# Kernel tuning notes

Measured on AMD Instinct MI355X. Metric: run time of the kernel, lower is better.

The kernel has to match this reference:

```python
import math
import jax, jax.numpy as jnp
import numpy as np
from jax import lax

jax.config.update("jax_enable_x64", True)

DECOMP_LEVEL = 5
# Daubechies-5 (db5) decomposition low-pass filter (pywt convention)
_DB5_LO = np.array([0.003335725285001549, -0.012580751999015526, -0.006241490213011705,
                    0.07757149384006515, -0.03224486958502952, -0.24229488706619015,
                    0.13842814590110342, 0.7243085284385744, 0.6038292697974729,
                    0.160102397974125], dtype=np.float64)
_L = _DB5_LO.size
_DB5_HI = _DB5_LO[::-1].copy() * ((-1.0) ** np.arange(_L))  # QMF high-pass
LO = jnp.asarray(_DB5_LO, jnp.float32)
HI = jnp.asarray(_DB5_HI, jnp.float32)
LOR = jnp.asarray(_DB5_LO[::-1].copy(), jnp.float32)
HIR = jnp.asarray(_DB5_HI[::-1].copy(), jnp.float32)


def _an_last(x):
    # orthonormal periodized analysis along last axis: (..., n) -> (..., n/2) x2
    n = x.shape[-1]
    lead = x.shape[:-1]
    xp = jnp.concatenate([x, x[..., : _L - 2]], axis=-1).reshape(-1, 1, n + _L - 2)
    k = jnp.stack([LO, HI])[:, None, :]  # (2,1,L)
    y = lax.conv_general_dilated(xp, k, (2,), "VALID")  # (B,2,n/2)
    y = y.reshape(lead + (2, n // 2))
    return y[..., 0, :], y[..., 1, :]


def _syn_last(a, d):
    # exact transpose/inverse of _an_last (orthonormal -> W^T = W^-1)
    n2 = a.shape[-1]
    n = 2 * n2
    lead = a.shape[:-1]
    B = int(np.prod(lead)) if lead else 1
    u = jnp.zeros((B, 2, n), a.dtype)
    u = u.at[:, 0, ::2].set(a.reshape(B, n2))
    u = u.at[:, 1, ::2].set(d.reshape(B, n2))
    up = jnp.concatenate([u[..., -(_L - 1):], u], axis=-1)  # circular left pad
    k = jnp.stack([LOR, HIR])[None, :, :]  # (1,2,L)
    y = lax.conv_general_dilated(up, k, (1,), "VALID")  # (B,1,n)
    return y.reshape(lead + (n,))


def _dwt2(x):  # x: (C,h,w) -> ll, lh, hl, hh each (C,h/2,w/2)
    a_h, d_h = _an_last(x.swapaxes(-1, -2))
    a_h = a_h.swapaxes(-1, -2)
    d_h = d_h.swapaxes(-1, -2)
    ll, lh = _an_last(a_h)
    hl, hh = _an_last(d_h)
    return ll, lh, hl, hh


def _idwt2(ll, lh, hl, hh):
    a_h = _syn_last(ll, lh)
    d_h = _syn_last(hl, hh)
    return _syn_last(a_h.swapaxes(-1, -2), d_h.swapaxes(-1, -2)).swapaxes(-1, -2)


def _estimate_noise(data):
    p = data.shape[0]
    rr = data @ data.T
    rri = jnp.linalg.inv(rr + 1e-6 * jnp.eye(p, dtype=data.dtype))
    def per_band(i):
        xx = rri - jnp.outer(rri[:, i], rri[i, :]) / rri[i, i]
        beta = xx @ rr[:, i]
        return beta.at[i].set(0.0)
    betas = jax.vmap(per_band)(jnp.arange(p))  # (p,p)
    return data - betas @ data


def hyres_forward(x):
    H, W, K = x.shape
    N = H * W
    data = x.reshape(N, K).T.astype(jnp.float64)
    w = _estimate_noise(data)
    omega1 = (jnp.sqrt(jnp.var(w, axis=1, ddof=1)) + 1e-30) ** 2  # (K,) f64
    y_w = x * omega1 ** -0.5  # whitened, f64
    u, s, v_pca = jnp.linalg.svd(y_w.reshape(N, K), full_matrices=False)
    pc = (u * s).reshape(W, H, K).astype(jnp.float32).transpose(2, 0, 1)  # (K,H,W)
    # multi-level 2D DWT per channel
    ll = pc
    highs = []
    for _ in range(DECOMP_LEVEL):
        ll, lh, hl, hh = _dwt2(ll)
        highs.append((lh, hl, hh))
    # overwrite-style full coefficient image [[LL,LH],[HL,HH]] recursively
    full = ll
    for lh, hl, hh in reversed(highs):
        top = jnp.concatenate([full, lh], axis=-1)
        bot = jnp.concatenate([hl, hh], axis=-1)
        full = jnp.concatenate([top, bot], axis=-2)
    V = full.transpose(1, 2, 0).reshape(N, K)
    V2 = V * V
    norm_v = jnp.sum(V2)
    n_xyz = jnp.asarray(V.size, jnp.float32)
    col_norm = jnp.sum(V2, axis=0)  # (K,)
    # SURE of soft-threshold over a 15-point grid in [0, sqrt(log N)]
    ts = np.linspace(0.0, math.sqrt(math.log(N)), 15).astype(np.float32)
    sure_cols = []
    for t in ts:
        t2 = float(t * t)
        s_t = (jnp.sum(jnp.minimum(V2, t2), axis=0)
               + 2.0 * jnp.sum((V2 > t2).astype(jnp.float32), axis=0)
               - col_norm)
        sure_cols.append(s_t)
    sure_all = jnp.stack(sure_cols, axis=1)  # (K,15)
    c_const = norm_v - n_xyz
    # replicate the in-place cumulative update: S_r = sum_{j<r} S_j + sure_r + C
    def step(acc, sure_r):
        s_r = acc + sure_r + c_const
        return acc + s_r, jnp.min(s_r)
    _, min_sure = lax.scan(step, jnp.zeros((15,), jnp.float32), sure_all)
    # early-exit: first rank>1 where min_sure increases; else loop ends at K-1
    cond = min_sure[2:] > min_sure[1:-1]
    rank = jnp.where(jnp.any(cond), 2 + jnp.argmax(cond), K - 1)
    mask = (jnp.arange(K) < rank).astype(jnp.float32)[:, None, None]
    # truncation-to-rank == zeroing channels >= rank (inverse DWT is linear)
    y = ll * mask
    for lh, hl, hh in reversed(highs):
        y = _idwt2(y, lh * mask, hl * mask, hh * mask)
    y_est = y.transpose(1, 2, 0).reshape(N, K)  # zero cols beyond rank
    out = (omega1.astype(jnp.float32) ** 0.5) * (y_est @ v_pca.astype(jnp.float32)).reshape(H, W, K)
    return out


def setup_inputs() -> dict:
    key = jax.random.key(0)
    k1, k2, k3 = jax.random.split(key, 3)
    H = W = 384
    K = 191
    R = 8  # low-rank spectral structure + noise, as HyRes assumes
    a = jax.random.normal(k1, (H * W, R), jnp.float32)
    b = jax.random.normal(k2, (R, K), jnp.float32)
    x = (a @ b) / np.sqrt(R) + 0.1 * jax.random.normal(k3, (H * W, K), jnp.float32)
    return {"x": x.reshape(H, W, K)}


def reference(x):
    return hyres_forward(x)
```

## Files before the change

### kernel.cpp

```cpp
#include <hip/hip_runtime.h>
#include <math.h>

#define K_     191
#define LD     192
#define N_     147456
#define MSUB   16
#define NT     15
#define TRI_N  18336
#define SMEM_CHOL  ((TRI_N + 1056) * 8)
#define SMEM_SOLVE ((TRI_N + 192 + 192 + 192) * 8)
#define SMEM2_SZ (6880 * 8 + 32 * 4 + TRI_N * 4)

#define NPAIR  6
#define NSPLIT 256
#define CHUNK  (N_ / NSPLIT)
#define RSTEP  16

__constant__ float c_lo[10] = {
  0.003335725285001549f, -0.012580751999015526f, -0.006241490213011705f,
  0.07757149384006515f,  -0.03224486958502952f, -0.24229488706619015f,
  0.13842814590110342f,   0.7243085284385744f,   0.6038292697974729f,
  0.160102397974125f };
__constant__ float c_hi[10] = {
  0.160102397974125f,    -0.6038292697974729f,   0.7243085284385744f,
 -0.13842814590110342f,  -0.24229488706619015f,  0.03224486958502952f,
  0.07757149384006515f,   0.006241490213011705f,-0.012580751999015526f,
 -0.003335725285001549f };

__global__ __launch_bounds__(256, 6) void k_rr(const float* __restrict__ x,
                                               double* __restrict__ rrg,
                                               double* __restrict__ m)
{
  __shared__ float Asf[2][RSTEP][64];
  __shared__ float Bsf[2][RSTEP][64];

  const int bid   = blockIdx.x;
  const int split = bid & (NSPLIT - 1);
  const int pair  = bid >> 8;
  const int BI[6] = {0, 0, 0, 1, 1, 2};
  const int BJ[6] = {0, 1, 2, 1, 2, 2};
  const int bi = BI[pair], bj = BJ[pair];
  const int diag = (bi == bj);
  const int ca = bi * 64, cb = bj * 64;

  const int t  = threadIdx.x;
  const int tx = t & 15, ty = t >> 4;
  const int mycol = t & 63, rowgrp = t >> 6;
  const long n0 = (long)split * CHUNK;

  double acc[4][4];
  #pragma unroll
  for (int v = 0; v < 4; ++v)
    #pragma unroll
    for (int u = 0; u < 4; ++u) acc[v][u] = 0.0;
  double csum = 0.0;

  float ra[4], rbv[4];
  const int cA = ca + mycol, cB = cb + mycol;
  const bool okA = (cA < K_), okB = (cB < K_);

  auto LOADT = [&](int r0) {
    #pragma unroll
    for (int i = 0; i < 4; ++i) {
      int row = i * 4 + rowgrp;
      long gr = (n0 + r0 + row) * (long)K_;
      float va = okA ? x[gr + cA] : 0.f;
      ra[i] = va;
      if (diag) csum += (double)va;
      else      rbv[i] = okB ? x[gr + cB] : 0.f;
    }
  };
  auto WRITET = [&](int buf) {
    #pragma unroll
    for (int i = 0; i < 4; ++i) {
      int row = i * 4 + rowgrp;
      Asf[buf][row][mycol] = ra[i];
      if (!diag) Bsf[buf][row][mycol] = rbv[i];
    }
  };

  LOADT(0);
  WRITET(0);
  __syncthreads();

  int cur = 0;
  for (int r0 = 0; r0 < CHUNK; r0 += RSTEP) {
    const bool hasnext = (r0 + RSTEP < CHUNK);
    if (hasnext) LOADT(r0 + RSTEP);
    const float (*As)[64] = Asf[cur];
    const float (*Bs)[64] = diag ? Asf[cur] : Bsf[cur];
    #pragma unroll 4
    for (int k = 0; k < RSTEP; ++k) {
      double a0 = (double)As[k][ty],      a1 = (double)As[k][ty + 16];
      double a2 = (double)As[k][ty + 32], a3 = (double)As[k][ty + 48];
      double b0 = (double)Bs[k][tx],      b1 = (double)Bs[k][tx + 16];
      double b2 = (double)Bs[k][tx + 32], b3 = (double)Bs[k][tx + 48];
      acc[0][0] += a0 * b0; acc[0][1] += a0 * b1; acc[0][2] += a0 * b2; acc[0][3] += a0 * b3;
      acc[1][0] += a1 * b0; acc[1][1] += a1 * b1; acc[1][2] += a1 * b2; acc[1][3] += a1 * b3;
      acc[2][0] += a2 * b0; acc[2][1] += a2 * b1; acc[2][2] += a2 * b2; acc[2][3] += a2 * b3;
      acc[3][0] += a3 * b0; acc[3][1] += a3 * b1; acc[3][2] += a3 * b2; acc[3][3] += a3 * b3;
    }
    if (hasnext) WRITET(cur ^ 1);
    __syncthreads();
    cur ^= 1;
  }

  #pragma unroll
  for (int v = 0; v < 4; ++v) {
    int mrow = ca + ty + 16 * v;
    #pragma unroll
    for (int u = 0; u < 4; ++u) {
      int ncol = cb + tx + 16 * u;
      if (mrow < K_ && ncol < K_)
        atomicAdd(&rrg[(size_t)mrow * K_ + ncol], acc[v][u]);
    }
  }

  if (diag) {
    double* sc = (double*)Bsf;
    sc[t] = csum;
    __syncthreads();
    if (t < 64) {
      int c = ca + t;
      if (c < K_) {
        double s = sc[t] + sc[t + 64] + sc[t + 128] + sc[t + 192];
        atomicAdd(&m[c], s);
      }
    }
  }
}

__global__ __launch_bounds__(256) void k_reduce(const double* __restrict__ rrg,
                                                double* __restrict__ rr)
{
  int idx = blockIdx.x * 256 + threadIdx.x;
  if (idx >= TRI_N) return;
  int i = (int)((sqrtf(8.f * (float)idx + 1.f) - 1.f) * 0.5f);
  while ((i + 1) * (i + 2) / 2 <= idx) ++i;
  while (i * (i + 1) / 2 > idx) --i;
  int j = idx - (i * (i + 1)) / 2;
  double s = rrg[(size_t)j * K_ + i];
  rr[i * LD + j] = s;
  rr[j * LD + i] = s;
}

__global__ __launch_bounds__(512) void k_chol(
    const double* __restrict__ rr, double* __restrict__ Lg,
    double* __restrict__ rdg)
{
  extern __shared__ double smem[];
  double* tri = smem;
  double* tmp = smem + TRI_N;
  const int t = threadIdx.x;

  for (int i = t >> 5; i < K_; i += 16) {
    int base = (i * (i + 1)) / 2;
    for (int j = t & 31; j <= i; j += 32) {
      double v = rr[i * LD + j];
      tri[base + j] = (i == j) ? v + 1e-6 : v;
    }
  }
  __syncthreads();

  for (int J = 0; J < 6; ++J) {
    const int j0 = J * 32;
    const int nb = (K_ - j0 < 32) ? (K_ - j0) : 32;

    if (t < 64) {
      const int rl = t & 31;
      double a[32];
      #pragma unroll
      for (int c = 0; c < 32; ++c) {
        int i = j0 + rl;
        a[c] = (c <= rl && rl < nb) ? tri[(i * (i + 1)) / 2 + j0 + c] : 0.0;
      }
      #pragma unroll
      for (int k = 0; k < 32; ++k) {
        double akk = __shfl(a[k], k);
        double piv = sqrt(akk);
        double inv = 1.0 / piv;
        if (t == k) {
          tmp[k] = inv;
          if (j0 + k < K_) rdg[j0 + k] = inv;
        }
        a[k] = (rl == k) ? piv : a[k] * inv;
        #pragma unroll
        for (int c = k + 1; c < 32; ++c) {
          double lck = __shfl(a[k], c);
          if (c <= rl) a[c] -= a[k] * lck;
        }
      }
      if (t < 32 && rl < nb) {
        int i = j0 + rl;
        int rb = (i * (i + 1)) / 2 + j0;
        #pragma unroll
        for (int c = 0; c < 32; ++c)
          if (c <= rl) tri[rb + c] = a[c];
      }
    }
    __syncthreads();

    {
      int p = j0 + 32 + t;
      if (nb == 32 && p < K_) {
        int pb = (p * (p + 1)) / 2 + j0;
        double v[32];
        #pragma unroll
        for (int c = 0; c < 32; ++c) v[c] = tri[pb + c];
        #pragma unroll
        for (int c = 0; c < 32; ++c) {
          double s = v[c];
          #pragma unroll
          for (int q = 0; q < c; ++q) {
            int cc = j0 + c;
            s -= v[q] * tri[(cc * (cc + 1)) / 2 + j0 + q];
          }
          v[c] = s * tmp[c];
        }
        #pragma unroll
        for (int c = 0; c < 32; ++c) tri[pb + c] = v[c];
      }
    }
    __syncthreads();

    {
      int s0 = j0 + 32;
      int n = K_ - s0;
      if (n > 0) {
        int R4 = (n + 3) >> 2;
        int T4 = R4 * (R4 + 1) / 2;
        for (int tile = t; tile < T4; tile += 512) {
          int ti = (int)((sqrtf(8.f * (float)tile + 1.f) - 1.f) * 0.5f);
          while ((ti + 1) * (ti + 2) / 2 <= tile) ++ti;
          while (ti * (ti + 1) / 2 > tile) --ti;
          int tj = tile - ti * (ti + 1) / 2;
          int r0 = s0 + ti * 4, c0 = s0 + tj * 4;
          int rb[4], cb[4];
          #pragma unroll
          for (int u = 0; u < 4; ++u) {
            int r = (r0 + u < K_) ? r0 + u : K_ - 1;
            rb[u] = (r * (r + 1)) / 2;
            int c = (c0 + u < K_) ? c0 + u : K_ - 1;
            cb[u] = (c * (c + 1)) / 2;
          }
          double acc[4][4];
          #pragma unroll
          for (int u = 0; u < 4; ++u)
            #pragma unroll
            for (int v2 = 0; v2 < 4; ++v2) acc[u][v2] = 0.0;
          #pragma unroll 4
          for (int p = 0; p < 32; ++p) {
            double lr[4], lc[4];
            #pragma unroll
            for (int u = 0; u < 4; ++u) {
              lr[u] = tri[rb[u] + j0 + p];
              lc[u] = tri[cb[u] + j0 + p];
            }
            #pragma unroll
            for (int u = 0; u < 4; ++u)
              #pragma unroll
              for (int v2 = 0; v2 < 4; ++v2) acc[u][v2] += lr[u] * lc[v2];
          }
          #pragma unroll
          for (int u = 0; u < 4; ++u) {
            int r = r0 + u;
            if (r < K_) {
              #pragma unroll
              for (int v2 = 0; v2 < 4; ++v2) {
                int c = c0 + v2;
                if (c <= r) tri[rb[u] + c] -= acc[u][v2];
              }
            }
          }
        }
      }
    }
    __syncthreads();
  }

  for (int idx = t; idx < TRI_N; idx += 512) Lg[idx] = tri[idx];
}

__global__ __launch_bounds__(256) void k_csolve(
    const double* __restrict__ Lg, const double* __restrict__ rdg,
    const double* __restrict__ mg, double* __restrict__ s2g,
    double* __restrict__ zg)
{
  extern __shared__ double ssm[];
  double* Ls   = ssm;
  double* rd_s = Ls + TRI_N;
  double* m_sh = rd_s + 192;
  double* ys   = m_sh + 192;
  const int t = threadIdx.x;
  const int bid = blockIdx.x;

  const int start = (bid < K_) ? (bid * (bid + 1)) / 2 : 0;
  for (int idx = start + t; idx < TRI_N; idx += 256) Ls[idx] = Lg[idx];
  if (t < K_) { rd_s[t] = rdg[t]; m_sh[t] = mg[t]; }
  __syncthreads();

  if (t >= 64) return;
  const int l = t;

  if (bid < K_) {
    const int i = bid;
    double x0 = 0.0, x1 = 0.0, x2 = 0.0;
    {
      double rdi = rd_s[i];
      if ((i & 63) == l) {
        int sl = i >> 6;
        if (sl == 0) x0 = rdi; else if (sl == 1) x1 = rdi; else x2 = rdi;
      }
    }
    for (int r = i + 1; r < K_; ++r) {
      int rb = (r * (r + 1)) >> 1;
      double partial = 0.0;
      { int k = l;       if (k < r) partial += Ls[rb + k] * x0; }
      { int k = l + 64;  if (k < r) partial += Ls[rb + k] * x1; }
      { int k = l + 128; if (k < r) partial += Ls[rb + k] * x2; }
      #pragma unroll
      for (int mm = 32; mm > 0; mm >>= 1) partial += __shfl_xor(partial, mm);
      double val = -partial * rd_s[r];
      if ((r & 63) == l) {
        int sl = r >> 6;
        if (sl == 0) x0 = val; else if (sl == 1) x1 = val; else x2 = val;
      }
    }
    double s2p = x0 * x0 + x1 * x1 + x2 * x2;
    #pragma unroll
    for (int mm = 32; mm > 0; mm >>= 1) s2p += __shfl_xor(s2p, mm);
    if (l == 0) s2g[i] = s2p;
  } else {
    double y0 = 0.0, y1 = 0.0, y2 = 0.0;
    for (int r = 0; r < K_; ++r) {
      int rb = (r * (r + 1)) >> 1;
      double partial = 0.0;
      { int k = l;       if (k < r) partial += Ls[rb + k] * y0; }
      { int k = l + 64;  if (k < r) partial += Ls[rb + k] * y1; }
      { int k = l + 128; if (k < r) partial += Ls[rb + k] * y2; }
      #pragma unroll
      for (int mm = 32; mm > 0; mm >>= 1) partial += __shfl_xor(partial, mm);
      double val = (m_sh[r] - partial) * rd_s[r];
      if ((r & 63) == l) {
        int sl = r >> 6;
        if (sl == 0) y0 = val; else if (sl == 1) y1 = val; else y2 = val;
      }
      if (l == 0) ys[r] = val;
    }
    double z0 = 0.0, z1 = 0.0, z2 = 0.0;
    for (int r = K_ - 1; r >= 0; --r) {
      double partial = 0.0;
      { int k = l;       if (k > r && k < K_) partial += Ls[((k * (k + 1)) >> 1) + r] * z0; }
      { int k = l + 64;  if (k > r && k < K_) partial += Ls[((k * (k + 1)) >> 1) + r] * z1; }
      { int k = l + 128; if (k > r && k < K_) partial += Ls[((k * (k + 1)) >> 1) + r] * z2; }
      #pragma unroll
      for (int mm = 32; mm > 0; mm >>= 1) partial += __shfl_xor(partial, mm);
      double val = (ys[r] - partial) * rd_s[r];
      if ((r & 63) == l) {
        int sl = r >> 6;
        if (sl == 0) z0 = val; else if (sl == 1) z1 = val; else z2 = val;
      }
      if (l == 0) zg[r] = val;
    }
  }
}

__global__ __launch_bounds__(256) void k_finals(
    const double* __restrict__ rr, const double* __restrict__ s2g,
    const double* __restrict__ zg, double* __restrict__ invsq,
    float* __restrict__ normv)
{
  __shared__ double tmps[K_];
  const int t = threadIdx.x;
  if (t < K_) {
    double dii = s2g[t];
    double q = 1.0 / dii;
    double sm_ = zg[t] / dii;
    double var = (q - sm_ * sm_ / (double)N_) / (double)(N_ - 1);
    double t1 = sqrt(var) + 1e-30;
    double om = t1 * t1;
    invsq[t] = 1.0 / sqrt(om);
    tmps[t] = rr[t * LD + t] / om;
  }
  __syncthreads();
  if (t < 64) {
    double s = 0.0;
    for (int i = t; i < K_; i += 64) s += tmps[i];
    #pragma unroll
    for (int off = 32; off > 0; off >>= 1) s += __shfl_down(s, off);
    if (t == 0) *normv = (float)s;
  }
}

__device__ __forceinline__ void cholqr(double* shQ, double* shS, int t)
{
  if (t < MSUB * MSUB) {
    int a = t & (MSUB - 1), b = t >> 4;
    double s = 0.0;
    for (int r = 0; r < K_; ++r) s += shQ[r * MSUB + a] * shQ[r * MSUB + b];
    shS[b * 17 + a] = s;
  }
  __syncthreads();
  for (int k = 0; k < MSUB; ++k) {
    if (t == 0) shS[k * 17 + k] = sqrt(shS[k * 17 + k]);
    __syncthreads();
    if (t > k && t < MSUB) shS[t * 17 + k] /= shS[k * 17 + k];
    __syncthreads();
    if (t < MSUB * MSUB) {
      int r = t & (MSUB - 1), c = t >> 4;
      if (c > k && r >= c) shS[r * 17 + c] -= shS[r * 17 + k] * shS[c * 17 + k];
    }
    __syncthreads();
  }
  if (t < K_) {
    double q[MSUB];
    #pragma unroll
    for (int c = 0; c < MSUB; ++c) {
      double v = shQ[t * MSUB + c];
      for (int p = 0; p < c; ++p) v -= q[p] * shS[c * 17 + p];
      q[c] = v / shS[c * 17 + c];
    }
    #pragma unroll
    for (int c = 0; c < MSUB; ++c) shQ[t * MSUB + c] = q[c];
  }
  __syncthreads();
}

__global__ __launch_bounds__(512) void k_sub(
    const double* __restrict__ rr, const double* __restrict__ invsq,
    float* __restrict__ W1, float* __restrict__ W2)
{
  extern __shared__ double dsm[];
  double* shQ  = dsm;
  double* shZ  = shQ + 3056;
  double* shS  = shZ + 3056;
  double* Ws   = shS + 272;
  double* inv_s= Ws + 272;
  double* ev   = inv_s + 192;
  double* cs_  = ev + 16;
  double* sn_  = cs_ + 8;
  int* ipp  = (int*)(sn_ + 8);
  int* iqq  = ipp + 8;
  int* perm = iqq + 8;
  float* tri = (float*)(perm + 16);
  const int t = threadIdx.x;

  if (t < K_) inv_s[t] = invsq[t];
  __syncthreads();
  for (int i = t >> 4; i < K_; i += 32) {
    int base = (i * (i + 1)) / 2;
    double di = inv_s[i];
    for (int j = t & 15; j <= i; j += 16)
      tri[base + j] = (float)(rr[i * LD + j] * di * inv_s[j]);
  }
  __syncthreads();

  for (int idx = t; idx < K_ * MSUB; idx += 512) {
    int i = idx >> 4, c = idx & 15;
    float g = (i >= c) ? tri[(i * (i + 1)) / 2 + c] : tri[(c * (c + 1)) / 2 + i];
    shQ[idx] = (double)g;
  }
  __syncthreads();

  cholqr(shQ, shS, t);
  for (int it = 0; it < 4; ++it) {
    for (int idx = t; idx < K_ * MSUB; idx += 512) shZ[idx] = shQ[idx];
    __syncthreads();
    if (t < 96 * 4) {
      int i2 = t >> 2, c4 = t & 3;
      int r0 = 2 * i2, r1 = r0 + 1;
      int has1 = (r1 < K_);
      int rb0 = (r0 * (r0 + 1)) >> 1;
      int rb1 = has1 ? ((r1 * (r1 + 1)) >> 1) : rb0;
      int cb0 = c4 * 4;
      double s0a = 0.0, s0b = 0.0, s0c = 0.0, s0d = 0.0;
      double s1a = 0.0, s1b = 0.0, s1c = 0.0, s1d = 0.0;
      #pragma unroll 2
      for (int k = 0; k <= r0; ++k) {
        double g0 = (double)tri[rb0 + k];
        double g1 = (double)tri[rb1 + k];
        double za = shZ[k * MSUB + cb0],     zb = shZ[k * MSUB + cb0 + 1];
        double zc = shZ[k * MSUB + cb0 + 2], zd = shZ[k * MSUB + cb0 + 3];
        s0a += g0 * za; s0b += g0 * zb; s0c += g0 * zc; s0d += g0 * zd;
        s1a += g1 * za; s1b += g1 * zb; s1c += g1 * zc; s1d += g1 * zd;
      }
      if (has1) {
        double g0 = (double)tri[rb1 + r0];
        double g1 = (double)tri[rb1 + r1];
        double za = shZ[r1 * MSUB + cb0],     zb = shZ[r1 * MSUB + cb0 + 1];
        double zc = shZ[r1 * MSUB + cb0 + 2], zd = shZ[r1 * MSUB + cb0 + 3];
        s0a += g0 * za; s0b += g0 * zb; s0c += g0 * zc; s0d += g0 * zd;
        s1a += g1 * za; s1b += g1 * zb; s1c += g1 * zc; s1d += g1 * zd;
      }
      int kk = ((r1 + 1) * (r1 + 2)) >> 1;
      #pragma unroll 2
      for (int k = r1 + 1; k < K_; ++k) {
        double g0 = (double)tri[kk + r0];
        double g1 = (double)tri[kk + r1];
        double za = shZ[k * MSUB + cb0],     zb = shZ[k * MSUB + cb0 + 1];
        double zc = shZ[k * MSUB + cb0 + 2], zd = shZ[k * MSUB + cb0 + 3];
        s0a += g0 * za; s0b += g0 * zb; s0c += g0 * zc; s0d += g0 * zd;
        s1a += g1 * za; s1b += g1 * zb; s1c += g1 * zc; s1d += g1 * zd;
        kk += k + 1;
      }
      shQ[r0 * MSUB + cb0]     = s0a;
      shQ[r0 * MSUB + cb0 + 1] = s0b;
      shQ[r0 * MSUB + cb0 + 2] = s0c;
      shQ[r0 * MSUB + cb0 + 3] = s0d;
      if (has1) {
        shQ[r1 * MSUB + cb0]     = s1a;
        shQ[r1 * MSUB + cb0 + 1] = s1b;
        shQ[r1 * MSUB + cb0 + 2] = s1c;
        shQ[r1 * MSUB + cb0 + 3] = s1d;
      }
    }
    __syncthreads();
    if (it < 3) cholqr(shQ, shS, t);
  }
  if (t < MSUB * MSUB) {
    int a = t & 15, b = t >> 4;
    double s = 0.0;
    for (int r = 0; r < K_; ++r) s += shZ[r * MSUB + b] * shQ[r * MSUB + a];
    shS[b * 17 + a] = s;
  }
  if (t < MSUB * 17) Ws[t] = 0.0;
  __syncthreads();
  if (t < MSUB) Ws[t * 17 + t] = 1.0;
  __syncthreads();
  for (int sweep = 0; sweep < 6; ++sweep) {
    for (int round = 0; round < 15; ++round) {
      if (t < 8) {
        int ia = (t == 0) ? 0 : (1 + ((t - 1 + round) % 15));
        int ib = 1 + ((14 - t + round) % 15);
        int p = ia < ib ? ia : ib;
        int q = ia < ib ? ib : ia;
        double app = shS[p * 17 + p], aqq = shS[q * 17 + q], apq = shS[p * 17 + q];
        double c = 1.0, s = 0.0;
        if (fabs(apq) > 1e-30 * (fabs(app) + fabs(aqq)) && apq != 0.0) {
          double tau = (aqq - app) / (2.0 * apq);
          double tt = (tau >= 0.0 ? 1.0 : -1.0) / (fabs(tau) + sqrt(1.0 + tau * tau));
          c = 1.0 / sqrt(1.0 + tt * tt); s = tt * c;
        }
        cs_[t] = c; sn_[t] = s; ipp[t] = p; iqq[t] = q;
      }
      __syncthreads();
      if (t < 128) {
        int i = t & 15, mI = t >> 4;
        int p = ipp[mI], q = iqq[mI];
        double c = cs_[mI], s = sn_[mI];
        double u = shS[i * 17 + p], v = shS[i * 17 + q];
        shS[i * 17 + p] = c * u - s * v; shS[i * 17 + q] = s * u + c * v;
        double wu = Ws[i * 17 + p], wv = Ws[i * 17 + q];
        Ws[i * 17 + p] = c * wu - s * wv; Ws[i * 17 + q] = s * wu + c * wv;
      }
      __syncthreads();
      if (t < 128) {
        int j = t & 15, mI = t >> 4;
        int p = ipp[mI], q = iqq[mI];
        double c = cs_[mI], s = sn_[mI];
        double u = shS[p * 17 + j], v = shS[q * 17 + j];
        shS[p * 17 + j] = c * u - s * v; shS[q * 17 + j] = s * u + c * v;
      }
      __syncthreads();
    }
  }
  if (t == 0) {
    for (int i = 0; i < MSUB; ++i) { ev[i] = shS[i * 17 + i]; perm[i] = i; }
    for (int i = 0; i < MSUB; ++i) {
      int best = i;
      for (int j = i + 1; j < MSUB; ++j)
        if (ev[perm[j]] > ev[perm[best]]) best = j;
      int tp = perm[i]; perm[i] = perm[best]; perm[best] = tp;
    }
  }
  __syncthreads();
  for (int idx = t; idx < K_ * MSUB; idx += 512) {
    int i = idx >> 4, c = idx & 15;
    int pc_ = perm[c];
    double e = 0.0;
    #pragma unroll
    for (int p = 0; p < MSUB; ++p) e += shZ[i * MSUB + p] * Ws[p * 17 + pc_];
    W1[i * MSUB + c] = (float)(inv_s[i] * e);
    W2[c * K_ + i]   = (float)(e / inv_s[i]);
  }
}

__global__ __launch_bounds__(256) void k_pc(const float* __restrict__ x,
                                            const float* __restrict__ W1,
                                            float* __restrict__ pc)
{
  __shared__ float xs[32][192];
  __shared__ float w1s[K_ * MSUB];
  int t = threadIdx.x;
  long n0 = (long)blockIdx.x * 32;
  for (int idx = t; idx < K_ * MSUB; idx += 256) w1s[idx] = W1[idx];
  for (int idx = t; idx < 32 * K_; idx += 256) {
    int row = idx / K_, col = idx - row * K_;
    xs[row][col] = x[(n0 + row) * K_ + col];
  }
  __syncthreads();
  int c = t & 15, nl = t >> 4;
  float a0 = 0.f, a1 = 0.f;
  for (int k = 0; k < K_; ++k) {
    float w = w1s[k * MSUB + c];
    a0 += xs[nl][k] * w;
    a1 += xs[nl + 16][k] * w;
  }
  __syncthreads();
  float* ts = &xs[0][0];
  ts[c * 33 + nl]      = a0;
  ts[c * 33 + nl + 16] = a1;
  __syncthreads();
  for (int idx = t; idx < MSUB * 32; idx += 256) {
    int cc = idx >> 5, nn = idx & 31;
    pc[(size_t)cc * N_ + n0 + nn] = ts[cc * 33 + nn];
  }
}

__global__ __launch_bounds__(256) void k_dwtv(const float* __restrict__ in,
                                              float* __restrict__ outv, int s)
{
  long gid = (long)blockIdx.x * 256 + threadIdx.x;
  int h = s >> 1;
  long per = (long)h * s;
  if (gid >= MSUB * per) return;
  int ch = (int)(gid / per);
  long rem = gid - (long)ch * per;
  int r = (int)(rem / s);
  int col = (int)(rem - (long)r * s);
  const float* cin = in + (long)ch * s * s;
  float la = 0.f, ld_ = 0.f;
  int base = 2 * r;
  #pragma unroll
  for (int l = 0; l < 10; ++l) {
    int rr_ = base + l; if (rr_ >= s) rr_ -= s;
    float v = cin[(long)rr_ * s + col];
    la += c_lo[l] * v; ld_ += c_hi[l] * v;
  }
  float* cout = outv + (long)ch * s * s;
  cout[(long)r * s + col] = la;
  cout[(long)(h + r) * s + col] = ld_;
}

__global__ __launch_bounds__(256) void k_dwth(const float* __restrict__ inv,
                                              float* __restrict__ llout,
                                              float* __restrict__ coef,
                                              int s, long offL, int last)
{
  long gid = (long)blockIdx.x * 256 + threadIdx.x;
  int h = s >> 1;
  long per = (long)s * h;
  if (gid >= MSUB * per) return;
  int ch = (int)(gid / per);
  long rem = gid - (long)ch * per;
  int r = (int)(rem / h);
  int mcol = (int)(rem - (long)r * h);
  const float* row = inv + (long)ch * s * s + (long)r * s;
  float lo = 0.f, hi = 0.f;
  int base = 2 * mcol;
  #pragma unroll
  for (int l = 0; l < 10; ++l) {
    int cc = base + l; if (cc >= s) cc -= s;
    float v = row[cc];
    lo += c_lo[l] * v; hi += c_hi[l] * v;
  }
  float* cslab = coef + (size_t)ch * N_ + offL;
  if (r < h) {
    llout[(size_t)ch * h * h + (long)r * h + mcol] = lo;
    if (last) coef[(size_t)ch * N_ + 147312 + (long)r * h + mcol] = lo;
    cslab[(long)r * h + mcol] = hi;
  } else {
    int rd = r - h;
    cslab[(long)h * h + (long)rd * h + mcol] = lo;
    cslab[(long)2 * h * h + (long)rd * h + mcol] = hi;
  }
}

__global__ __launch_bounds__(256) void k_stats(const float* __restrict__ coef,
                                               float* __restrict__ stats)
{
  int ch = blockIdx.x;
  int t = threadIdx.x;
  float T2[NT];
  {
    double stop = sqrt(log(147456.0));
    double step = stop / 14.0;
    for (int i = 0; i < NT; ++i) {
      double td = (i == 14) ? stop : (double)i * step;
      float tf = (float)td;
      T2[i] = tf * tf;
    }
  }
  float cn = 0.f, sm[NT], ct[NT];
  #pragma unroll
  for (int i = 0; i < NT; ++i) { sm[i] = 0.f; ct[i] = 0.f; }
  const float* base = coef + (size_t)ch * N_;
  for (int idx = t; idx < N_; idx += 256) {
    float v = base[idx];
    float v2 = v * v;
    cn += v2;
    #pragma unroll
    for (int i = 0; i < NT; ++i) {
      sm[i] += fminf(v2, T2[i]);
      ct[i] += (v2 > T2[i]) ? 1.0f : 0.0f;
    }
  }
  __shared__ float red2[4][32];
  int lane = t & 63, wv = t >> 6;
  for (int a = 0; a < 31; ++a) {
    float val = (a == 0) ? cn : ((a < 16) ? sm[a - 1] : ct[a - 16]);
    #pragma unroll
    for (int off = 32; off > 0; off >>= 1) val += __shfl_down(val, off);
    if (lane == 0) red2[wv][a] = val;
  }
  __syncthreads();
  if (t < 31)
    stats[ch * 31 + t] = red2[0][t] + red2[1][t] + red2[2][t] + red2[3][t];
}

__global__ void k_rank(const float* __restrict__ stats,
                       const float* __restrict__ normv, int* __restrict__ rankp)
{
  if (threadIdx.x != 0 || blockIdx.x != 0) return;
  float c_const = *normv - 28164096.0f;
  float acc[NT];
  for (int i = 0; i < NT; ++i) acc[i] = 0.f;
  float minsure[MSUB];
  for (int r = 0; r < MSUB; ++r) {
    float cn = stats[r * 31 + 0];
    float mn = 3.4e38f;
    for (int i = 0; i < NT; ++i) {
      float sure = stats[r * 31 + 1 + i] + 2.0f * stats[r * 31 + 16 + i] - cn;
      float s_r = acc[i] + sure + c_const;
      acc[i] = acc[i] + s_r;
      if (s_r < mn) mn = s_r;
    }
    minsure[r] = mn;
  }
  int rank = -1;
  for (int r = 2; r < MSUB; ++r) {
    if (minsure[r] > minsure[r - 1]) { rank = r; break; }
  }
  if (rank < 0) rank = MSUB - 1;
  *rankp = rank;
}

__global__ __launch_bounds__(256) void k_out(const float* __restrict__ pc,
                                             const float* __restrict__ W2,
                                             const int* __restrict__ rankp,
                                             float* __restrict__ out)
{
  long gid = (long)blockIdx.x * 256 + threadIdx.x;
  int n = (int)(gid / K_);
  int j = (int)(gid - (long)n * K_);
  int rank = *rankp;
  float acc = 0.f;
  for (int c = 0; c < rank; ++c)
    acc += pc[(size_t)c * N_ + n] * W2[c * K_ + j];
  out[gid] = acc;
}

extern "C" void kernel_launch(void* const* d_in, const int* in_sizes, int n_in,
                              void* d_out, int out_size, void* d_ws, size_t ws_size,
                              hipStream_t stream)
{
  if (n_in < 1 || in_sizes[0] != N_ * K_) return;
  const float* x = (const float*)d_in[0];
  float* out = (float*)d_out;
  (void)out_size;

  char* w = (char*)d_ws;
  size_t off = 0;
  auto alloc = [&](size_t bytes) -> char* {
    char* p = w + off;
    off = (off + bytes + 255) & ~(size_t)255;
    return p;
  };
  double* m_    = (double*)alloc(K_ * 8);
  double* rrp   = (double*)alloc((size_t)K_ * K_ * 8);
  double* rr    = (double*)alloc((size_t)K_ * LD * 8);
  double* Lg    = (double*)alloc((size_t)TRI_N * 8);
  double* rdg   = (double*)alloc(192 * 8);
  double* s2g   = (double*)alloc(192 * 8);
  double* zg    = (double*)alloc(192 * 8);
  double* invsq = (double*)alloc(K_ * 8);
  float*  normv = (float*)alloc(256);
  float*  W1    = (float*)alloc((size_t)K_ * MSUB * 4);
  float*  W2    = (float*)alloc((size_t)MSUB * K_ * 4);
  float*  pc    = (float*)alloc((size_t)MSUB * N_ * 4);
  float*  tmpv  = (float*)alloc((size_t)MSUB * N_ * 4);
  float*  coef  = (float*)alloc((size_t)MSUB * N_ * 4);
  float*  curA  = (float*)alloc((size_t)MSUB * 192 * 192 * 4);
  float*  curB  = (float*)alloc((size_t)MSUB * 96 * 96 * 4);
  float*  stats = (float*)alloc((size_t)MSUB * 31 * 4);
  int*    rankp = (int*)alloc(256);
  if (off > ws_size) return;

  hipMemsetAsync(m_, 0, K_ * sizeof(double), stream);
  hipMemsetAsync(rrp, 0, (size_t)K_ * K_ * sizeof(double), stream);

  hipFuncSetAttribute(reinterpret_cast<const void*>(k_chol),
                      hipFuncAttributeMaxDynamicSharedMemorySize, SMEM_CHOL);
  hipFuncSetAttribute(reinterpret_cast<const void*>(k_csolve),
                      hipFuncAttributeMaxDynamicSharedMemorySize, SMEM_SOLVE);
  hipFuncSetAttribute(reinterpret_cast<const void*>(k_sub),
                      hipFuncAttributeMaxDynamicSharedMemorySize, SMEM2_SZ);

  k_rr<<<NPAIR * NSPLIT, 256, 0, stream>>>(x, rrp, m_);
  k_reduce<<<(TRI_N + 255) / 256, 256, 0, stream>>>(rrp, rr);
  k_chol<<<1, 512, SMEM_CHOL, stream>>>(rr, Lg, rdg);
  k_csolve<<<K_ + 1, 256, SMEM_SOLVE, stream>>>(Lg, rdg, m_, s2g, zg);
  k_finals<<<1, 256, 0, stream>>>(rr, s2g, zg, invsq, normv);
  k_sub<<<1, 512, SMEM2_SZ, stream>>>(rr, invsq, W1, W2);
  k_pc<<<N_ / 32, 256, 0, stream>>>(x, W1, pc);

  int   sizes[5] = {384, 192, 96, 48, 24};
  long  offs[5]  = {0, 110592, 138240, 145152, 146880};
  float* lls[5]  = {curA, curB, curA, curB, curA};
  const float* curin = pc;
  for (int lev = 0; lev < 5; ++lev) {
    int s = sizes[lev], h = s >> 1;
    long nth = (long)MSUB * h * s;
    k_dwtv<<<(int)((nth + 255) / 256), 256, 0, stream>>>(curin, tmpv, s);
    k_dwth<<<(int)((nth + 255) / 256), 256, 0, stream>>>(tmpv, lls[lev], coef,
                                                         s, offs[lev],
                                                         lev == 4 ? 1 : 0);
    curin = lls[lev];
  }

  k_stats<<<MSUB, 256, 0, stream>>>(coef, stats);
  k_rank<<<1, 64, 0, stream>>>(stats, normv, rankp);
  k_out<<<(N_ * K_) / 256, 256, 0, stream>>>(pc, W2, rankp, out);
}
```

Before: 1.387 ms.

## Invert diagonal Cholesky block for panel solve and double rr reduction splits

```diff
diff --git a/kernel.cpp b/kernel.cpp
--- a/kernel.cpp
+++ b/kernel.cpp
@@ -7,12 +7,12 @@
 #define MSUB   16
 #define NT     15
 #define TRI_N  18336
-#define SMEM_CHOL  ((TRI_N + 1056) * 8)
+#define SMEM_CHOL  ((TRI_N + 1056 + 64) * 8)
 #define SMEM_SOLVE ((TRI_N + 192 + 192 + 192) * 8)
 #define SMEM2_SZ (6880 * 8 + 32 * 4 + TRI_N * 4)
 
 #define NPAIR  6
-#define NSPLIT 256
+#define NSPLIT 512
 #define CHUNK  (N_ / NSPLIT)
 #define RSTEP  16
 
@@ -27,7 +27,7 @@
   0.07757149384006515f,   0.006241490213011705f,-0.012580751999015526f,
  -0.003335725285001549f };
 
-__global__ __launch_bounds__(256, 6) void k_rr(const float* __restrict__ x,
+__global__ __launch_bounds__(256, 8) void k_rr(const float* __restrict__ x,
                                                double* __restrict__ rrg,
                                                double* __restrict__ m)
 {
@@ -36,7 +36,7 @@
 
   const int bid   = blockIdx.x;
   const int split = bid & (NSPLIT - 1);
-  const int pair  = bid >> 8;
+  const int pair  = bid >> 9;
   const int BI[6] = {0, 0, 0, 1, 1, 2};
   const int BJ[6] = {0, 1, 2, 1, 2, 2};
   const int bi = BI[pair], bj = BJ[pair];
@@ -149,8 +149,9 @@
     double* __restrict__ rdg)
 {
   extern __shared__ double smem[];
-  double* tri = smem;
-  double* tmp = smem + TRI_N;
+  double* tri  = smem;
+  double* tmp  = smem + TRI_N;
+  double* tmp2 = tmp + 1056;
   const int t = threadIdx.x;
 
   for (int i = t >> 5; i < K_; i += 16) {
@@ -180,7 +181,7 @@
         double piv = sqrt(akk);
         double inv = 1.0 / piv;
         if (t == k) {
-          tmp[k] = inv;
+          tmp2[k] = inv;
           if (j0 + k < K_) rdg[j0 + k] = inv;
         }
         a[k] = (rl == k) ? piv : a[k] * inv;
@@ -198,27 +199,40 @@
           if (c <= rl) tri[rb + c] = a[c];
       }
     }
+    if (t < 32) {
+      const int c = t;
+      double xcol[32];
+      #pragma unroll
+      for (int r = 0; r < 32; ++r) {
+        int rr_ = (j0 + r < K_) ? j0 + r : K_ - 1;
+        int rb2 = (rr_ * (rr_ + 1)) / 2 + j0;
+        double s = (r == c) ? 1.0 : 0.0;
+        #pragma unroll
+        for (int k = 0; k < 32; ++k)
+          if (k < r) s -= tri[rb2 + k] * xcol[k];
+        xcol[r] = s * tmp2[r];
+      }
+      #pragma unroll
+      for (int r = 0; r < 32; ++r)
+        tmp[r * 33 + c] = (r >= c) ? xcol[r] : 0.0;
+    }
     __syncthreads();
 
     {
       int p = j0 + 32 + t;
       if (nb == 32 && p < K_) {
         int pb = (p * (p + 1)) / 2 + j0;
-        double v[32];
+        double arow[32];
         #pragma unroll
-        for (int c = 0; c < 32; ++c) v[c] = tri[pb + c];
+        for (int k = 0; k < 32; ++k) arow[k] = tri[pb + k];
         #pragma unroll
         for (int c = 0; c < 32; ++c) {
-          double s = v[c];
+          double s = 0.0;
           #pragma unroll
-          for (int q = 0; q < c; ++q) {
-            int cc = j0 + c;
-            s -= v[q] * tri[(cc * (cc + 1)) / 2 + j0 + q];
-          }
-          v[c] = s * tmp[c];
+          for (int k = 0; k < 32; ++k)
+            if (k <= c) s += arow[k] * tmp[c * 33 + k];
+          tri[pb + c] = s;
         }
-        #pragma unroll
-        for (int c = 0; c < 32; ++c) tri[pb + c] = v[c];
       }
     }
     __syncthreads();
```

New measurement: 1.543 ms. 1.11x slower.
